# Kernel tuning notes

Hardware: AMD Instinct MI355X
Metric: run time of the kernel (lower is better)

The kernel has to match this reference:

```python
import jax, jax.numpy as jnp
import numpy as np

B, T, C = 1, 2048, 1024
H = 16
HD = C // H  # 64
K = 8
EPS = 1e-6
NEG = -1.0e9


def apply_rotary_emb(x, cos, sin):
    # x: (B,T,H,HD), cos/sin: (T, HD//2)
    x1, x2 = jnp.split(x, 2, axis=-1)
    c = cos[None, :, None, :]
    s = sin[None, :, None, :]
    return jnp.concatenate([x1 * c - x2 * s, x1 * s + x2 * c], axis=-1)


def rms_norm(x):
    return x * jax.lax.rsqrt(jnp.mean(jnp.square(x), axis=-1, keepdims=True) + EPS)


def setup_inputs() -> dict:
    key = jax.random.key(0)
    ks = jax.random.split(key, 8)
    x = jax.random.normal(ks[0], (B, T, C), dtype=jnp.float32)
    # standard RoPE tables
    inv_freq = 1.0 / (10000.0 ** (np.arange(0, HD, 2, dtype=np.float32) / HD))
    t = np.arange(T, dtype=np.float32)
    freqs = np.outer(t, inv_freq)  # (T, HD//2)
    cos = jnp.asarray(np.cos(freqs), dtype=jnp.float32)
    sin = jnp.asarray(np.sin(freqs), dtype=jnp.float32)
    std = 0.02
    Wq = std * jax.random.normal(ks[1], (C, C), dtype=jnp.float32)
    Wk = std * jax.random.normal(ks[2], (C, C), dtype=jnp.float32)
    Wv = std * jax.random.normal(ks[3], (C, C), dtype=jnp.float32)
    Wproj = std * jax.random.normal(ks[4], (C, C), dtype=jnp.float32)
    Wdq = jax.random.normal(ks[5], (C, K), dtype=jnp.float32) / np.sqrt(C)
    Wdk = jax.random.normal(ks[6], (C, K), dtype=jnp.float32) / np.sqrt(C)
    return {"x": x, "cos": cos, "sin": sin, "Wq": Wq, "Wk": Wk, "Wv": Wv,
            "Wproj": Wproj, "Wdq": Wdq, "Wdk": Wdk}


def reference(x, cos, sin, Wq, Wk, Wv, Wproj, Wdq, Wdk):
    b, t, c = x.shape
    q = (x @ Wq).reshape(b, t, H, HD)
    k = (x @ Wk).reshape(b, t, H, HD)
    v = (x @ Wv).reshape(b, t, H, HD)
    q = rms_norm(apply_rotary_emb(q, cos, sin))
    k = rms_norm(apply_rotary_emb(k, cos, sin))

    # digit projections (identical for every head in the source module)
    qd = x @ Wdq  # (B,T,K)
    kd = x @ Wdk  # (B,T,K)
    matches = qd[:, :, None, :] == kd[:, None, :, :]  # (B,Tq,Tk,K)
    prefix = jnp.cumprod(matches.astype(jnp.int32), axis=-1)
    lcp = jnp.sum(prefix, axis=-1)  # (B,Tq,Tk)
    lcp_mask = lcp >= (K - 1)

    causal = jnp.tril(jnp.ones((t, t), dtype=bool))
    combined = causal[None, None, :, :] & lcp_mask[:, None, :, :]  # (B,1->H,Tq,Tk)

    scale = 1.0 / jnp.sqrt(jnp.asarray(HD, x.dtype))
    scores = jnp.einsum('bqhd,bkhd->bhqk', q * scale, k)
    scores = jnp.where(combined, scores, NEG)
    w = jax.nn.softmax(scores, axis=-1)
    y = jnp.einsum('bhqk,bkhd->bqhd', w, v).reshape(b, t, c)
    return y @ Wproj
```

## Files before the change

### kernel.cpp

```cpp
#include <hip/hip_runtime.h>
#include <math.h>

#define T_DIM 2048
#define C_DIM 1024
#define H_NUM 16
#define HD_DIM 64
#define K_LCP 8
#define NEG_VAL -1.0e9f

typedef __bf16 bf16;
typedef __bf16 bf16x4 __attribute__((ext_vector_type(4)));
typedef __bf16 bf16x8 __attribute__((ext_vector_type(8)));
typedef float f32x4 __attribute__((ext_vector_type(4)));

__device__ void matvec_body(const float* __restrict__ vin, int npart,
                            const float* __restrict__ W, float* __restrict__ vout,
                            float scale, int blk) {
  __shared__ float xm[C_DIM];
  __shared__ float red[4][64];
  const int t = threadIdx.x;
  f32x4 s = {0.f, 0.f, 0.f, 0.f};
  if (npart) {
    for (int g = 0; g < npart; ++g) s += ((const f32x4*)vin)[g * 256 + t];
  } else {
    s = ((const f32x4*)vin)[t];
  }
  s *= scale;
  *(f32x4*)&xm[t * 4] = s;
  __syncthreads();
  const int j = blk * 64 + (t & 63);
  const int p = t >> 6;
  float acc = 0.f;
  for (int c = p * 256; c < p * 256 + 256; ++c)
    acc = fmaf(xm[c], W[(size_t)c * C_DIM + j], acc);
  red[p][t & 63] = acc;
  __syncthreads();
  if (t < 64)
    vout[blk * 64 + t] = (red[0][t] + red[1][t]) + (red[2][t] + red[3][t]);
}

__global__ __launch_bounds__(256) void fused_a(const float* __restrict__ x,
                                               const float* __restrict__ Wdq,
                                               const float* __restrict__ Wdk,
                                               bf16* __restrict__ xb,
                                               float* __restrict__ qd,
                                               float* __restrict__ kd,
                                               float* __restrict__ partial,
                                               int* __restrict__ flags) {
  const int tid = threadIdx.x;
  if (blockIdx.x >= 512) {
    const int b = blockIdx.x - 512;
    if (b == 0 && tid < 116) flags[tid] = 0;
    f32x4 s = {0.f, 0.f, 0.f, 0.f};
    for (int r = 0; r < 64; ++r)
      s += ((const f32x4*)(x + (size_t)(b * 64 + r) * C_DIM))[tid];
    ((f32x4*)(partial + (size_t)b * C_DIM))[tid] = s;
    return;
  }
  const int wave = tid >> 6, lane = tid & 63;
  const int t = blockIdx.x * 4 + wave;
  const float* xp = x + (size_t)t * C_DIM;
  bf16* xbp = xb + (size_t)t * C_DIM;
  float aq[8] = {}, ak[8] = {};
#pragma unroll
  for (int i = 0; i < 16; ++i) {
    const int c = i * 64 + lane;
    float xv = xp[c];
    xbp[c] = (bf16)xv;
    float4 wq0 = *(const float4*)(Wdq + (size_t)c * K_LCP);
    float4 wq1 = *(const float4*)(Wdq + (size_t)c * K_LCP + 4);
    float4 wk0 = *(const float4*)(Wdk + (size_t)c * K_LCP);
    float4 wk1 = *(const float4*)(Wdk + (size_t)c * K_LCP + 4);
    aq[0] = fmaf(xv, wq0.x, aq[0]); aq[1] = fmaf(xv, wq0.y, aq[1]);
    aq[2] = fmaf(xv, wq0.z, aq[2]); aq[3] = fmaf(xv, wq0.w, aq[3]);
    aq[4] = fmaf(xv, wq1.x, aq[4]); aq[5] = fmaf(xv, wq1.y, aq[5]);
    aq[6] = fmaf(xv, wq1.z, aq[6]); aq[7] = fmaf(xv, wq1.w, aq[7]);
    ak[0] = fmaf(xv, wk0.x, ak[0]); ak[1] = fmaf(xv, wk0.y, ak[1]);
    ak[2] = fmaf(xv, wk0.z, ak[2]); ak[3] = fmaf(xv, wk0.w, ak[3]);
    ak[4] = fmaf(xv, wk1.x, ak[4]); ak[5] = fmaf(xv, wk1.y, ak[5]);
    ak[6] = fmaf(xv, wk1.z, ak[6]); ak[7] = fmaf(xv, wk1.w, ak[7]);
  }
#pragma unroll
  for (int j = 0; j < 8; ++j) {
#pragma unroll
    for (int off = 32; off >= 1; off >>= 1) {
      aq[j] += __shfl_xor(aq[j], off);
      ak[j] += __shfl_xor(ak[j], off);
    }
  }
  if (lane == 0) {
    *(float4*)(qd + (size_t)t * K_LCP) = make_float4(aq[0], aq[1], aq[2], aq[3]);
    *(float4*)(qd + (size_t)t * K_LCP + 4) = make_float4(aq[4], aq[5], aq[6], aq[7]);
    *(float4*)(kd + (size_t)t * K_LCP) = make_float4(ak[0], ak[1], ak[2], ak[3]);
    *(float4*)(kd + (size_t)t * K_LCP + 4) = make_float4(ak[4], ak[5], ak[6], ak[7]);
  }
}

__global__ __launch_bounds__(256) void fused_b(
    const float* __restrict__ qd, const float* __restrict__ kd,
    const float* __restrict__ partial, const float* __restrict__ Wv,
    int* __restrict__ tilemask, int* __restrict__ allmask,
    float* __restrict__ vmean, int* __restrict__ qneed, int* __restrict__ kneed,
    int* __restrict__ vneed, int* __restrict__ vtneed, int* __restrict__ pneed,
    int* __restrict__ wneed) {
  const int tid = threadIdx.x;
  if (blockIdx.x >= 128) {
    matvec_body(partial, 32, Wv, vmean, 1.0f / 2048.0f, blockIdx.x - 128);
    return;
  }
  const int qb = blockIdx.x;
  __shared__ float qds[16][K_LCP];
  __shared__ int tm[32];
  if (tid < 32) tm[tid] = 0;
  if (tid < 16 * K_LCP)
    qds[tid >> 3][tid & 7] = qd[(size_t)(qb * 16 + (tid >> 3)) * K_LCP + (tid & 7)];
  __syncthreads();
  for (int key = tid; key < T_DIM; key += 256) {
    float kv[K_LCP];
    *(float4*)&kv[0] = *(const float4*)(kd + (size_t)key * K_LCP);
    *(float4*)&kv[4] = *(const float4*)(kd + (size_t)key * K_LCP + 4);
    int any = 0;
#pragma unroll
    for (int ql = 0; ql < 16; ++ql) {
      int qg = qb * 16 + ql;
      if (key > qg) continue;
      int lcp = 0;
#pragma unroll
      for (int jj = 0; jj < K_LCP; ++jj) {
        if (qds[ql][jj] == kv[jj]) lcp++;
        else break;
      }
      if (lcp >= K_LCP - 1) any = 1;
    }
    if (any) tm[key >> 6] = 1;
  }
  __syncthreads();
  int anytm = 0;
#pragma unroll
  for (int i = 0; i < 32; ++i) anytm |= tm[i];
  if (tid < 32) tilemask[qb * 32 + tid] = tm[tid];
  if (tid == 0) allmask[qb] = !anytm;
  if (anytm) {
    if (tid < 32) {
      if (tm[tid]) {
        atomicOr(&kneed[tid >> 1], 1);
        atomicOr(&vneed[tid >> 1], 1);
      } else {
        atomicOr(&vtneed[tid], 1);
        atomicOr(&vneed[tid >> 1], 1);
      }
    }
    if (tid == 0) {
      atomicOr(&qneed[qb >> 3], 1);
      atomicOr(&pneed[qb >> 2], 1);
      atomicOr(&wneed[0], 1);
      atomicOr(&wneed[1], 1);
      atomicOr(&wneed[2], 1);
      atomicOr(&wneed[3], 1);
    }
  }
}

__global__ __launch_bounds__(256) void fused_e(
    const float* __restrict__ vmean, const float* __restrict__ WprojF,
    float* __restrict__ rowout, const float* __restrict__ W0,
    const float* __restrict__ W1, const float* __restrict__ W2,
    const float* __restrict__ W3, bf16* __restrict__ O0, bf16* __restrict__ O1,
    bf16* __restrict__ O2, bf16* __restrict__ O3, const int* __restrict__ wneed) {
  if (blockIdx.x < 16) {
    matvec_body(vmean, 0, WprojF, rowout, 1.0f, blockIdx.x);
    return;
  }
  const int idx = blockIdx.x - 16;
  const int z = idx >> 8;
  if (!wneed[z]) return;
  const float* W = (z == 0) ? W0 : (z == 1) ? W1 : (z == 2) ? W2 : W3;
  bf16* O = (z == 0) ? O0 : (z == 1) ? O1 : (z == 2) ? O2 : O3;
  __shared__ bf16 tile[64][65];
  const int rem = idx & 255;
  const int bk = (rem >> 4) * 64;
  const int bn = (rem & 15) * 64;
  const int r = threadIdx.x >> 2;
  const int c0 = (threadIdx.x & 3) * 16;
  const float* src = W + (size_t)(bk + r) * C_DIM + bn + c0;
#pragma unroll
  for (int t = 0; t < 16; t += 4) {
    float4 f = *(const float4*)(src + t);
    tile[r][c0 + t + 0] = (bf16)f.x;
    tile[r][c0 + t + 1] = (bf16)f.y;
    tile[r][c0 + t + 2] = (bf16)f.z;
    tile[r][c0 + t + 3] = (bf16)f.w;
  }
  __syncthreads();
  bf16* dst = O + (size_t)(bn + r) * C_DIM + bk + c0;
#pragma unroll
  for (int t = 0; t < 16; ++t) dst[t] = tile[c0 + t][r];
}

template <int TMt, int MI, int NA>
__global__ __launch_bounds__(256) void gemm_bf16(
    const bf16* __restrict__ A, const bf16* __restrict__ Bt0,
    const bf16* __restrict__ Bt1, const bf16* __restrict__ Bt2, void* C0,
    void* C1, void* C2, int N, int Kd, int bf16_out,
    const float* __restrict__ cosT, const float* __restrict__ sinT,
    const int* __restrict__ fq, const int* __restrict__ fk,
    const int* __restrict__ fv, float* __restrict__ vtsum,
    const float* __restrict__ rowout, int mode) {
  if (!mode && blockIdx.z == 1) {
    const int b = blockIdx.y * 8 + blockIdx.x;
    f32x4 v = ((const f32x4*)rowout)[threadIdx.x];
#pragma unroll
    for (int r = 0; r < 8; ++r) {
      const int row = b * 8 + r;
      if (fq[row >> 6]) continue;
      ((f32x4*)((float*)C0 + (size_t)row * C_DIM))[threadIdx.x] = v;
    }
    return;
  }
  if (mode) {
    const int* f = (blockIdx.z == 0) ? fq : (blockIdx.z == 1) ? fk : fv;
    if (!f[blockIdx.y]) return;
  } else {
    if (!fq[blockIdx.y]) return;
  }
  const bf16* Bt = (blockIdx.z == 0) ? Bt0 : (blockIdx.z == 1) ? Bt1 : Bt2;
  __shared__ __align__(16) bf16 As[TMt * 32];
  __shared__ __align__(16) bf16 Bs[128 * 32];
  const int tid = threadIdx.x;
  const int bm = blockIdx.y * TMt;
  const int bn = blockIdx.x * 128;
  const int wave = tid >> 6, lane = tid & 63;
  const int lr = lane >> 2;
  const int lc = (lane & 3) * 8;
  bf16* gA = (bf16*)(A + (size_t)(bm + wave * 16 * NA + lr) * Kd + lc);
  bf16* gB = (bf16*)(Bt + (size_t)(bn + wave * 32 + lr) * Kd + lc);
  bf16* lA = As + wave * 512 * NA;
  bf16* lB = Bs + wave * 1024;
  const int wr = (wave >> 1) * (MI * 16);
  const int wc = (wave & 1) * 64;
  const int fm = lane & 15;
  const int fk_ = (lane >> 4) * 8;

  f32x4 acc[MI][4] = {};
  for (int k0 = 0; k0 < Kd; k0 += 32) {
    __syncthreads();
#pragma unroll
    for (int u = 0; u < NA; ++u)
      __builtin_amdgcn_global_load_lds(
          (__attribute__((address_space(1))) void*)(gA + (size_t)u * 16 * Kd + k0),
          (__attribute__((address_space(3))) void*)(lA + u * 512), 16, 0, 0);
#pragma unroll
    for (int u = 0; u < 2; ++u)
      __builtin_amdgcn_global_load_lds(
          (__attribute__((address_space(1))) void*)(gB + (size_t)u * 16 * Kd + k0),
          (__attribute__((address_space(3))) void*)(lB + u * 512), 16, 0, 0);
    __syncthreads();
    bf16x8 af[MI], bfr[4];
#pragma unroll
    for (int i = 0; i < MI; ++i)
      af[i] = *(const bf16x8*)(As + (size_t)(wr + i * 16 + fm) * 32 + fk_);
#pragma unroll
    for (int j = 0; j < 4; ++j)
      bfr[j] = *(const bf16x8*)(Bs + (size_t)(wc + j * 16 + fm) * 32 + fk_);
#pragma unroll
    for (int i = 0; i < MI; ++i)
#pragma unroll
      for (int j = 0; j < 4; ++j)
        acc[i][j] = __builtin_amdgcn_mfma_f32_16x16x32_bf16(af[i], bfr[j],
                                                            acc[i][j], 0, 0, 0);
  }
  const int cq = (lane >> 4) * 4;
  if (mode && blockIdx.z < 2) {
    bf16* C = (bf16*)((blockIdx.z == 0) ? C0 : C1);
#pragma unroll
    for (int i = 0; i < MI; ++i)
#pragma unroll
      for (int r = 0; r < 4; ++r) {
        const int t = bm + wr + i * 16 + cq + r;
        float c0 = cosT[(size_t)t * 32 + fm], s0 = sinT[(size_t)t * 32 + fm];
        float c1 = cosT[(size_t)t * 32 + 16 + fm], s1 = sinT[(size_t)t * 32 + 16 + fm];
        float a0 = acc[i][0][r], a1 = acc[i][1][r];
        float a2 = acc[i][2][r], a3 = acc[i][3][r];
        float o0 = a0 * c0 - a2 * s0, o2 = a0 * s0 + a2 * c0;
        float o1 = a1 * c1 - a3 * s1, o3 = a1 * s1 + a3 * c1;
        float ss = o0 * o0 + o1 * o1 + o2 * o2 + o3 * o3;
        ss += __shfl_xor(ss, 1);
        ss += __shfl_xor(ss, 2);
        ss += __shfl_xor(ss, 4);
        ss += __shfl_xor(ss, 8);
        float rn = 1.0f / sqrtf(ss * (1.0f / 64.0f) + 1e-6f);
        size_t base = (size_t)t * N + bn + wc + fm;
        C[base + 0] = (bf16)(o0 * rn);
        C[base + 16] = (bf16)(o1 * rn);
        C[base + 32] = (bf16)(o2 * rn);
        C[base + 48] = (bf16)(o3 * rn);
      }
  } else if (bf16_out) {
    bf16* C = (bf16*)((blockIdx.z == 0) ? C0 : (blockIdx.z == 1) ? C1 : C2);
#pragma unroll
    for (int i = 0; i < MI; ++i)
#pragma unroll
      for (int r = 0; r < 4; ++r) {
        size_t base = (size_t)(bm + wr + i * 16 + cq + r) * N + bn + wc + fm;
#pragma unroll
        for (int j = 0; j < 4; ++j) C[base + j * 16] = (bf16)acc[i][j][r];
      }
    if (mode && blockIdx.z == 2 && MI == 4) {
      const int kt = (bm + wr) >> 6;
#pragma unroll
      for (int j = 0; j < 4; ++j) {
        float s = 0.f;
#pragma unroll
        for (int i = 0; i < MI; ++i)
#pragma unroll
          for (int r = 0; r < 4; ++r) s += acc[i][j][r];
        s += __shfl_xor(s, 16);
        s += __shfl_xor(s, 32);
        if ((lane >> 4) == 0)
          vtsum[(size_t)kt * C_DIM + bn + wc + j * 16 + fm] = s;
      }
    }
  } else {
    float* C = (float*)((blockIdx.z == 0) ? C0 : (blockIdx.z == 1) ? C1 : C2);
#pragma unroll
    for (int i = 0; i < MI; ++i)
#pragma unroll
      for (int r = 0; r < 4; ++r) {
        size_t base = (size_t)(bm + wr + i * 16 + cq + r) * N + bn + wc + fm;
#pragma unroll
        for (int j = 0; j < 4; ++j) C[base + j * 16] = acc[i][j][r];
      }
  }
}

#define QT 16
#define KT 64

__global__ __launch_bounds__(256) void attn2(
    const bf16* __restrict__ q, const bf16* __restrict__ k,
    const bf16* __restrict__ v, const float* __restrict__ qd,
    const float* __restrict__ kd, const float* __restrict__ vtsum,
    const float* __restrict__ vmean, const int* __restrict__ tilemask,
    const int* __restrict__ allmask, const int* __restrict__ pneed,
    bf16* __restrict__ y) {
  const int h = blockIdx.y;
  const int qb = blockIdx.x;
  const int q0 = qb * QT;
  const int tid = threadIdx.x;
  const int q_l = tid >> 4;
  const int sub = tid & 15;

  if (allmask[qb]) {
    if (pneed[qb >> 2]) {
      f32x4 vm = *(const f32x4*)(vmean + h * HD_DIM + sub * 4);
      bf16x4 o = {(bf16)vm[0], (bf16)vm[1], (bf16)vm[2], (bf16)vm[3]};
      *(bf16x4*)(y + (size_t)(q0 + q_l) * C_DIM + h * HD_DIM + sub * 4) = o;
    }
    return;
  }

  __shared__ float qs[QT][HD_DIM];
  __shared__ float qds[QT][K_LCP];
  __shared__ float ks[KT][HD_DIM];
  __shared__ float vs[KT][HD_DIM];
  __shared__ float kds[KT][K_LCP];
  __shared__ float sc[QT][KT + 4];

  {
    int r = tid >> 4, c4 = (tid & 15) * 4;
    bf16x4 t4 = *(const bf16x4*)(q + (size_t)(q0 + r) * C_DIM + h * HD_DIM + c4);
    qs[r][c4 + 0] = (float)t4[0] * 0.125f;
    qs[r][c4 + 1] = (float)t4[1] * 0.125f;
    qs[r][c4 + 2] = (float)t4[2] * 0.125f;
    qs[r][c4 + 3] = (float)t4[3] * 0.125f;
    if (tid < QT * K_LCP)
      qds[tid >> 3][tid & 7] = qd[(size_t)(q0 + (tid >> 3)) * K_LCP + (tid & 7)];
  }
  __syncthreads();

  float m = -INFINITY;
  float l = 0.f;
  float acc[4] = {0.f, 0.f, 0.f, 0.f};

  for (int kt = 0; kt < T_DIM / KT; ++kt) {
    if (!tilemask[qb * 32 + kt]) {
      if (m <= NEG_VAL) {
        m = NEG_VAL;
        l += (float)KT;
        f32x4 vt = *(const f32x4*)(vtsum + (size_t)kt * C_DIM + h * HD_DIM + sub * 4);
        acc[0] += vt[0];
        acc[1] += vt[1];
        acc[2] += vt[2];
        acc[3] += vt[3];
      }
      continue;
    }
    const int k0 = kt * KT;
    __syncthreads();
#pragma unroll
    for (int it = 0; it < 4; ++it) {
      int i = tid + it * 256;
      int row = i >> 4, c4 = (i & 15) * 4;
      bf16x4 kv = *(const bf16x4*)(k + (size_t)(k0 + row) * C_DIM + h * HD_DIM + c4);
      bf16x4 vv = *(const bf16x4*)(v + (size_t)(k0 + row) * C_DIM + h * HD_DIM + c4);
      ks[row][c4 + 0] = (float)kv[0];
      ks[row][c4 + 1] = (float)kv[1];
      ks[row][c4 + 2] = (float)kv[2];
      ks[row][c4 + 3] = (float)kv[3];
      vs[row][c4 + 0] = (float)vv[0];
      vs[row][c4 + 1] = (float)vv[1];
      vs[row][c4 + 2] = (float)vv[2];
      vs[row][c4 + 3] = (float)vv[3];
    }
#pragma unroll
    for (int it = 0; it < 2; ++it) {
      int i = tid + it * 256;
      kds[i >> 3][i & 7] = kd[(size_t)(k0 + (i >> 3)) * K_LCP + (i & 7)];
    }
    __syncthreads();

    const int kb = sub * 4;
    bool msk[4];
#pragma unroll
    for (int j = 0; j < 4; ++j) {
      int kg = k0 + kb + j;
      int lcp = 0;
#pragma unroll
      for (int jj = 0; jj < K_LCP; ++jj) {
        if (qds[q_l][jj] == kds[kb + j][jj]) lcp++;
        else break;
      }
      msk[j] = (lcp >= K_LCP - 1) && (kg <= q0 + q_l);
    }
    float s[4] = {0.f, 0.f, 0.f, 0.f};
#pragma unroll
    for (int d4 = 0; d4 < 16; ++d4) {
      float4 q4 = *(const float4*)&qs[q_l][d4 * 4];
#pragma unroll
      for (int j = 0; j < 4; ++j) {
        float4 k4 = *(const float4*)&ks[kb + j][d4 * 4];
        s[j] = fmaf(q4.x, k4.x, s[j]);
        s[j] = fmaf(q4.y, k4.y, s[j]);
        s[j] = fmaf(q4.z, k4.z, s[j]);
        s[j] = fmaf(q4.w, k4.w, s[j]);
      }
    }
    float tmax = NEG_VAL;
#pragma unroll
    for (int j = 0; j < 4; ++j) {
      s[j] = msk[j] ? s[j] : NEG_VAL;
      tmax = fmaxf(tmax, s[j]);
    }
#pragma unroll
    for (int off = 1; off < 16; off <<= 1) tmax = fmaxf(tmax, __shfl_xor(tmax, off));
    float m_new = fmaxf(m, tmax);
    float alpha = expf(m - m_new);
    float lsum = 0.f;
#pragma unroll
    for (int j = 0; j < 4; ++j) {
      float p = expf(s[j] - m_new);
      sc[q_l][kb + j] = p;
      lsum += p;
    }
#pragma unroll
    for (int off = 1; off < 16; off <<= 1) lsum += __shfl_xor(lsum, off);
    l = l * alpha + lsum;
    m = m_new;
    acc[0] *= alpha;
    acc[1] *= alpha;
    acc[2] *= alpha;
    acc[3] *= alpha;
    __syncthreads();
#pragma unroll 8
    for (int kk = 0; kk < KT; ++kk) {
      float w = sc[q_l][kk];
      const float4 v4 = *(const float4*)&vs[kk][sub * 4];
      acc[0] = fmaf(w, v4.x, acc[0]);
      acc[1] = fmaf(w, v4.y, acc[1]);
      acc[2] = fmaf(w, v4.z, acc[2]);
      acc[3] = fmaf(w, v4.w, acc[3]);
    }
  }

  const float inv_l = 1.0f / l;
  bf16x4 o = {(bf16)(acc[0] * inv_l), (bf16)(acc[1] * inv_l),
              (bf16)(acc[2] * inv_l), (bf16)(acc[3] * inv_l)};
  *(bf16x4*)(y + (size_t)(q0 + q_l) * C_DIM + h * HD_DIM + sub * 4) = o;
}

extern "C" void kernel_launch(void* const* d_in, const int* in_sizes, int n_in,
                              void* d_out, int out_size, void* d_ws, size_t ws_size,
                              hipStream_t stream) {
  const float* x = (const float*)d_in[0];
  const float* cosT = (const float*)d_in[1];
  const float* sinT = (const float*)d_in[2];
  const float* Wq = (const float*)d_in[3];
  const float* Wk = (const float*)d_in[4];
  const float* Wv = (const float*)d_in[5];
  const float* Wproj = (const float*)d_in[6];
  const float* Wdq = (const float*)d_in[7];
  const float* Wdk = (const float*)d_in[8];
  float* out = (float*)d_out;

  char* ws = (char*)d_ws;
  const size_t TC2 = (size_t)T_DIM * C_DIM * 2;
  const size_t CC2 = (size_t)C_DIM * C_DIM * 2;
  bf16* xb = (bf16*)(ws + 0);
  bf16* wqt = (bf16*)(ws + TC2);
  bf16* wkt = (bf16*)(ws + TC2 + CC2);
  bf16* wvt = (bf16*)(ws + TC2 + 2 * CC2);
  bf16* wpt = (bf16*)(ws + TC2 + 3 * CC2);
  bf16* qb = (bf16*)(ws + TC2 + 4 * CC2);
  bf16* kb = (bf16*)(ws + 2 * TC2 + 4 * CC2);
  bf16* vb = (bf16*)(ws + 3 * TC2 + 4 * CC2);
  char* p2 = ws + 4 * TC2 + 4 * CC2;
  float* qd = (float*)p2;                      p2 += (size_t)T_DIM * K_LCP * 4;
  float* kd = (float*)p2;                      p2 += (size_t)T_DIM * K_LCP * 4;
  float* vtsum = (float*)p2;                   p2 += 32 * C_DIM * 4;
  float* vmean = (float*)p2;                   p2 += C_DIM * 4;
  float* partial = (float*)p2;                 p2 += 32 * C_DIM * 4;
  float* rowout = (float*)p2;                  p2 += C_DIM * 4;
  int* tilemask = (int*)p2;                    p2 += (T_DIM / 16) * 32 * 4;
  int* allmask = (int*)p2;                     p2 += (T_DIM / 16) * 4;
  int* qneed = (int*)p2;                       p2 += 16 * 4;
  int* kneed = (int*)p2;                       p2 += 16 * 4;
  int* vneed = (int*)p2;                       p2 += 16 * 4;
  int* vtneed = (int*)p2;                      p2 += 32 * 4;
  int* pneed = (int*)p2;                       p2 += 32 * 4;
  int* wneed = (int*)p2;                       p2 += 4 * 4;
  bf16* yb = xb;

  fused_a<<<544, 256, 0, stream>>>(x, Wdq, Wdk, xb, qd, kd, partial, qneed);
  fused_b<<<144, 256, 0, stream>>>(qd, kd, partial, Wv, tilemask, allmask,
                                   vmean, qneed, kneed, vneed, vtneed, pneed,
                                   wneed);
  fused_e<<<16 + 1024, 256, 0, stream>>>(vmean, Wproj, rowout, Wq, Wk, Wv,
                                         Wproj, wqt, wkt, wvt, wpt, wneed);
  gemm_bf16<128, 4, 2><<<dim3(C_DIM / 128, T_DIM / 128, 3), 256, 0, stream>>>(
      xb, wqt, wkt, wvt, qb, kb, vb, C_DIM, C_DIM, 1, cosT, sinT, qneed, kneed,
      vneed, vtsum, rowout, 1);
  attn2<<<dim3(T_DIM / QT, H_NUM), 256, 0, stream>>>(
      qb, kb, vb, qd, kd, vtsum, vmean, tilemask, allmask, pneed, yb);
  gemm_bf16<64, 2, 1><<<dim3(C_DIM / 128, T_DIM / 64, 2), 256, 0, stream>>>(
      yb, wpt, wpt, wpt, out, out, out, C_DIM, C_DIM, 0, cosT, sinT, pneed,
      pneed, pneed, vtsum, rowout, 0);
}
```

Measured before the change: 121.6 us.

## Fold weight transposes into first kernel and merge matvec into QKV GEMM launch

The four weight transpose-to-bf16 conversions move into the first kernel alongside the digit projections, so they no longer wait on the mask pass. The Wproj matvec is merged into the QKV GEMM launch, which cuts the chain from six kernels to five. In exchange, all four weights are now always converted, even when the mask would have skipped them, and the vtneed/wneed gating is dropped. The V-tile column sums are now always computed in the V GEMM.

```diff
diff --git a/kernel.cpp b/kernel.cpp
--- a/kernel.cpp
+++ b/kernel.cpp
@@ -13,86 +13,85 @@
 typedef __bf16 bf16x8 __attribute__((ext_vector_type(8)));
 typedef float f32x4 __attribute__((ext_vector_type(4)));
 
-__device__ void matvec_body(const float* __restrict__ vin, int npart,
-                            const float* __restrict__ W, float* __restrict__ vout,
-                            float scale, int blk) {
-  __shared__ float xm[C_DIM];
-  __shared__ float red[4][64];
-  const int t = threadIdx.x;
-  f32x4 s = {0.f, 0.f, 0.f, 0.f};
-  if (npart) {
-    for (int g = 0; g < npart; ++g) s += ((const f32x4*)vin)[g * 256 + t];
-  } else {
-    s = ((const f32x4*)vin)[t];
-  }
-  s *= scale;
-  *(f32x4*)&xm[t * 4] = s;
-  __syncthreads();
-  const int j = blk * 64 + (t & 63);
-  const int p = t >> 6;
-  float acc = 0.f;
-  for (int c = p * 256; c < p * 256 + 256; ++c)
-    acc = fmaf(xm[c], W[(size_t)c * C_DIM + j], acc);
-  red[p][t & 63] = acc;
-  __syncthreads();
-  if (t < 64)
-    vout[blk * 64 + t] = (red[0][t] + red[1][t]) + (red[2][t] + red[3][t]);
-}
-
-__global__ __launch_bounds__(256) void fused_a(const float* __restrict__ x,
-                                               const float* __restrict__ Wdq,
-                                               const float* __restrict__ Wdk,
-                                               bf16* __restrict__ xb,
-                                               float* __restrict__ qd,
-                                               float* __restrict__ kd,
-                                               float* __restrict__ partial,
-                                               int* __restrict__ flags) {
+__global__ __launch_bounds__(256) void fused_a(
+    const float* __restrict__ x, const float* __restrict__ Wdq,
+    const float* __restrict__ Wdk, const float* __restrict__ Wq,
+    const float* __restrict__ Wk, const float* __restrict__ Wv,
+    const float* __restrict__ Wproj, bf16* __restrict__ xb,
+    float* __restrict__ qd, float* __restrict__ kd, float* __restrict__ partial,
+    int* __restrict__ flags, bf16* __restrict__ wqt, bf16* __restrict__ wkt,
+    bf16* __restrict__ wvt, bf16* __restrict__ wpt) {
+  __shared__ bf16 tile[64][65];
+  const int vb = blockIdx.x;
   const int tid = threadIdx.x;
-  if (blockIdx.x >= 512) {
-    const int b = blockIdx.x - 512;
-    if (b == 0 && tid < 116) flags[tid] = 0;
+  if (vb < 512) {
+    const int wave = tid >> 6, lane = tid & 63;
+    const int t = vb * 4 + wave;
+    const float* xp = x + (size_t)t * C_DIM;
+    bf16* xbp = xb + (size_t)t * C_DIM;
+    float aq[8] = {}, ak[8] = {};
+#pragma unroll
+    for (int i = 0; i < 16; ++i) {
+      const int c = i * 64 + lane;
+      float xv = xp[c];
+      xbp[c] = (bf16)xv;
+      float4 wq0 = *(const float4*)(Wdq + (size_t)c * K_LCP);
+      float4 wq1 = *(const float4*)(Wdq + (size_t)c * K_LCP + 4);
+      float4 wk0 = *(const float4*)(Wdk + (size_t)c * K_LCP);
+      float4 wk1 = *(const float4*)(Wdk + (size_t)c * K_LCP + 4);
+      aq[0] = fmaf(xv, wq0.x, aq[0]); aq[1] = fmaf(xv, wq0.y, aq[1]);
+      aq[2] = fmaf(xv, wq0.z, aq[2]); aq[3] = fmaf(xv, wq0.w, aq[3]);
+      aq[4] = fmaf(xv, wq1.x, aq[4]); aq[5] = fmaf(xv, wq1.y, aq[5]);
+      aq[6] = fmaf(xv, wq1.z, aq[6]); aq[7] = fmaf(xv, wq1.w, aq[7]);
+      ak[0] = fmaf(xv, wk0.x, ak[0]); ak[1] = fmaf(xv, wk0.y, ak[1]);
+      ak[2] = fmaf(xv, wk0.z, ak[2]); ak[3] = fmaf(xv, wk0.w, ak[3]);
+      ak[4] = fmaf(xv, wk1.x, ak[4]); ak[5] = fmaf(xv, wk1.y, ak[5]);
+      ak[6] = fmaf(xv, wk1.z, ak[6]); ak[7] = fmaf(xv, wk1.w, ak[7]);
+    }
+#pragma unroll
+    for (int j = 0; j < 8; ++j) {
+#pragma unroll
+      for (int off = 32; off >= 1; off >>= 1) {
+        aq[j] += __shfl_xor(aq[j], off);
+        ak[j] += __shfl_xor(ak[j], off);
+      }
+    }
+    if (lane == 0) {
+      *(float4*)(qd + (size_t)t * K_LCP) = make_float4(aq[0], aq[1], aq[2], aq[3]);
+      *(float4*)(qd + (size_t)t * K_LCP + 4) = make_float4(aq[4], aq[5], aq[6], aq[7]);
+      *(float4*)(kd + (size_t)t * K_LCP) = make_float4(ak[0], ak[1], ak[2], ak[3]);
+      *(float4*)(kd + (size_t)t * K_LCP + 4) = make_float4(ak[4], ak[5], ak[6], ak[7]);
+    }
+  } else if (vb < 544) {
+    const int b = vb - 512;
+    if (b == 0 && tid < 112) flags[tid] = 0;
     f32x4 s = {0.f, 0.f, 0.f, 0.f};
     for (int r = 0; r < 64; ++r)
       s += ((const f32x4*)(x + (size_t)(b * 64 + r) * C_DIM))[tid];
     ((f32x4*)(partial + (size_t)b * C_DIM))[tid] = s;
-    return;
-  }
-  const int wave = tid >> 6, lane = tid & 63;
-  const int t = blockIdx.x * 4 + wave;
-  const float* xp = x + (size_t)t * C_DIM;
-  bf16* xbp = xb + (size_t)t * C_DIM;
-  float aq[8] = {}, ak[8] = {};
-#pragma unroll
-  for (int i = 0; i < 16; ++i) {
-    const int c = i * 64 + lane;
-    float xv = xp[c];
-    xbp[c] = (bf16)xv;
-    float4 wq0 = *(const float4*)(Wdq + (size_t)c * K_LCP);
-    float4 wq1 = *(const float4*)(Wdq + (size_t)c * K_LCP + 4);
-    float4 wk0 = *(const float4*)(Wdk + (size_t)c * K_LCP);
-    float4 wk1 = *(const float4*)(Wdk + (size_t)c * K_LCP + 4);
-    aq[0] = fmaf(xv, wq0.x, aq[0]); aq[1] = fmaf(xv, wq0.y, aq[1]);
-    aq[2] = fmaf(xv, wq0.z, aq[2]); aq[3] = fmaf(xv, wq0.w, aq[3]);
-    aq[4] = fmaf(xv, wq1.x, aq[4]); aq[5] = fmaf(xv, wq1.y, aq[5]);
-    aq[6] = fmaf(xv, wq1.z, aq[6]); aq[7] = fmaf(xv, wq1.w, aq[7]);
-    ak[0] = fmaf(xv, wk0.x, ak[0]); ak[1] = fmaf(xv, wk0.y, ak[1]);
-    ak[2] = fmaf(xv, wk0.z, ak[2]); ak[3] = fmaf(xv, wk0.w, ak[3]);
-    ak[4] = fmaf(xv, wk1.x, ak[4]); ak[5] = fmaf(xv, wk1.y, ak[5]);
-    ak[6] = fmaf(xv, wk1.z, ak[6]); ak[7] = fmaf(xv, wk1.w, ak[7]);
-  }
-#pragma unroll
-  for (int j = 0; j < 8; ++j) {
-#pragma unroll
-    for (int off = 32; off >= 1; off >>= 1) {
-      aq[j] += __shfl_xor(aq[j], off);
-      ak[j] += __shfl_xor(ak[j], off);
-    }
-  }
-  if (lane == 0) {
-    *(float4*)(qd + (size_t)t * K_LCP) = make_float4(aq[0], aq[1], aq[2], aq[3]);
-    *(float4*)(qd + (size_t)t * K_LCP + 4) = make_float4(aq[4], aq[5], aq[6], aq[7]);
-    *(float4*)(kd + (size_t)t * K_LCP) = make_float4(ak[0], ak[1], ak[2], ak[3]);
-    *(float4*)(kd + (size_t)t * K_LCP + 4) = make_float4(ak[4], ak[5], ak[6], ak[7]);
+  } else {
+    const int idx = vb - 544;
+    const int z = idx >> 8;
+    const float* W = (z == 0) ? Wq : (z == 1) ? Wk : (z == 2) ? Wv : Wproj;
+    bf16* O = (z == 0) ? wqt : (z == 1) ? wkt : (z == 2) ? wvt : wpt;
+    const int rem = idx & 255;
+    const int bk = (rem >> 4) * 64;
+    const int bn = (rem & 15) * 64;
+    const int r = tid >> 2;
+    const int c0 = (tid & 3) * 16;
+    const float* src = W + (size_t)(bk + r) * C_DIM + bn + c0;
+#pragma unroll
+    for (int t = 0; t < 16; t += 4) {
+      float4 f = *(const float4*)(src + t);
+      tile[r][c0 + t + 0] = (bf16)f.x;
+      tile[r][c0 + t + 1] = (bf16)f.y;
+      tile[r][c0 + t + 2] = (bf16)f.z;
+      tile[r][c0 + t + 3] = (bf16)f.w;
+    }
+    __syncthreads();
+    bf16* dst = O + (size_t)(bn + r) * C_DIM + bk + c0;
+#pragma unroll
+    for (int t = 0; t < 16; ++t) dst[t] = tile[c0 + t][r];
   }
 }
 
@@ -101,11 +100,27 @@
     const float* __restrict__ partial, const float* __restrict__ Wv,
     int* __restrict__ tilemask, int* __restrict__ allmask,
     float* __restrict__ vmean, int* __restrict__ qneed, int* __restrict__ kneed,
-    int* __restrict__ vneed, int* __restrict__ vtneed, int* __restrict__ pneed,
-    int* __restrict__ wneed) {
+    int* __restrict__ vneed, int* __restrict__ pneed) {
   const int tid = threadIdx.x;
   if (blockIdx.x >= 128) {
-    matvec_body(partial, 32, Wv, vmean, 1.0f / 2048.0f, blockIdx.x - 128);
+    __shared__ float xm[C_DIM];
+    __shared__ float red[4][64];
+    const int blk = blockIdx.x - 128;
+    f32x4 s = {0.f, 0.f, 0.f, 0.f};
+    for (int g = 0; g < 32; ++g) s += ((const f32x4*)partial)[g * 256 + tid];
+    s *= (1.0f / 2048.0f);
+    *(f32x4*)&xm[tid * 4] = s;
+    __syncthreads();
+    const int j = blk * 64 + (tid & 63);
+    const int p = tid >> 6;
+    float acc = 0.f;
+    for (int c = p * 256; c < p * 256 + 256; ++c)
+      acc = fmaf(xm[c], Wv[(size_t)c * C_DIM + j], acc);
+    red[p][tid & 63] = acc;
+    __syncthreads();
+    if (tid < 64)
+      vmean[blk * 64 + tid] =
+          (red[0][tid] + red[1][tid]) + (red[2][tid] + red[3][tid]);
     return;
   }
   const int qb = blockIdx.x;
@@ -142,93 +157,24 @@
   if (tid == 0) allmask[qb] = !anytm;
   if (anytm) {
     if (tid < 32) {
-      if (tm[tid]) {
-        atomicOr(&kneed[tid >> 1], 1);
-        atomicOr(&vneed[tid >> 1], 1);
-      } else {
-        atomicOr(&vtneed[tid], 1);
-        atomicOr(&vneed[tid >> 1], 1);
-      }
+      if (tm[tid]) atomicOr(&kneed[tid >> 1], 1);
+      atomicOr(&vneed[tid >> 1], 1);
     }
     if (tid == 0) {
       atomicOr(&qneed[qb >> 3], 1);
       atomicOr(&pneed[qb >> 2], 1);
-      atomicOr(&wneed[0], 1);
-      atomicOr(&wneed[1], 1);
-      atomicOr(&wneed[2], 1);
-      atomicOr(&wneed[3], 1);
-    }
-  }
-}
-
-__global__ __launch_bounds__(256) void fused_e(
-    const float* __restrict__ vmean, const float* __restrict__ WprojF,
-    float* __restrict__ rowout, const float* __restrict__ W0,
-    const float* __restrict__ W1, const float* __restrict__ W2,
-    const float* __restrict__ W3, bf16* __restrict__ O0, bf16* __restrict__ O1,
-    bf16* __restrict__ O2, bf16* __restrict__ O3, const int* __restrict__ wneed) {
-  if (blockIdx.x < 16) {
-    matvec_body(vmean, 0, WprojF, rowout, 1.0f, blockIdx.x);
-    return;
-  }
-  const int idx = blockIdx.x - 16;
-  const int z = idx >> 8;
-  if (!wneed[z]) return;
-  const float* W = (z == 0) ? W0 : (z == 1) ? W1 : (z == 2) ? W2 : W3;
-  bf16* O = (z == 0) ? O0 : (z == 1) ? O1 : (z == 2) ? O2 : O3;
-  __shared__ bf16 tile[64][65];
-  const int rem = idx & 255;
-  const int bk = (rem >> 4) * 64;
-  const int bn = (rem & 15) * 64;
-  const int r = threadIdx.x >> 2;
-  const int c0 = (threadIdx.x & 3) * 16;
-  const float* src = W + (size_t)(bk + r) * C_DIM + bn + c0;
-#pragma unroll
-  for (int t = 0; t < 16; t += 4) {
-    float4 f = *(const float4*)(src + t);
-    tile[r][c0 + t + 0] = (bf16)f.x;
-    tile[r][c0 + t + 1] = (bf16)f.y;
-    tile[r][c0 + t + 2] = (bf16)f.z;
-    tile[r][c0 + t + 3] = (bf16)f.w;
-  }
-  __syncthreads();
-  bf16* dst = O + (size_t)(bn + r) * C_DIM + bk + c0;
-#pragma unroll
-  for (int t = 0; t < 16; ++t) dst[t] = tile[c0 + t][r];
+    }
+  }
 }
 
 template <int TMt, int MI, int NA>
-__global__ __launch_bounds__(256) void gemm_bf16(
-    const bf16* __restrict__ A, const bf16* __restrict__ Bt0,
-    const bf16* __restrict__ Bt1, const bf16* __restrict__ Bt2, void* C0,
-    void* C1, void* C2, int N, int Kd, int bf16_out,
-    const float* __restrict__ cosT, const float* __restrict__ sinT,
-    const int* __restrict__ fq, const int* __restrict__ fk,
-    const int* __restrict__ fv, float* __restrict__ vtsum,
-    const float* __restrict__ rowout, int mode) {
-  if (!mode && blockIdx.z == 1) {
-    const int b = blockIdx.y * 8 + blockIdx.x;
-    f32x4 v = ((const f32x4*)rowout)[threadIdx.x];
-#pragma unroll
-    for (int r = 0; r < 8; ++r) {
-      const int row = b * 8 + r;
-      if (fq[row >> 6]) continue;
-      ((f32x4*)((float*)C0 + (size_t)row * C_DIM))[threadIdx.x] = v;
-    }
-    return;
-  }
-  if (mode) {
-    const int* f = (blockIdx.z == 0) ? fq : (blockIdx.z == 1) ? fk : fv;
-    if (!f[blockIdx.y]) return;
-  } else {
-    if (!fq[blockIdx.y]) return;
-  }
-  const bf16* Bt = (blockIdx.z == 0) ? Bt0 : (blockIdx.z == 1) ? Bt1 : Bt2;
-  __shared__ __align__(16) bf16 As[TMt * 32];
-  __shared__ __align__(16) bf16 Bs[128 * 32];
+__device__ void gemm_body(bf16* As, bf16* Bs, const bf16* A, const bf16* Bt,
+                          void* Cv, int bx, int by, int z, int mode,
+                          const float* cosT, const float* sinT, float* vtsum) {
   const int tid = threadIdx.x;
-  const int bm = blockIdx.y * TMt;
-  const int bn = blockIdx.x * 128;
+  const int Kd = C_DIM, N = C_DIM;
+  const int bm = by * TMt;
+  const int bn = bx * 128;
   const int wave = tid >> 6, lane = tid & 63;
   const int lr = lane >> 2;
   const int lc = (lane & 3) * 8;
@@ -270,15 +216,16 @@
                                                             acc[i][j], 0, 0, 0);
   }
   const int cq = (lane >> 4) * 4;
-  if (mode && blockIdx.z < 2) {
-    bf16* C = (bf16*)((blockIdx.z == 0) ? C0 : C1);
+  if (mode && z < 2) {
+    bf16* C = (bf16*)Cv;
 #pragma unroll
     for (int i = 0; i < MI; ++i)
 #pragma unroll
       for (int r = 0; r < 4; ++r) {
         const int t = bm + wr + i * 16 + cq + r;
         float c0 = cosT[(size_t)t * 32 + fm], s0 = sinT[(size_t)t * 32 + fm];
-        float c1 = cosT[(size_t)t * 32 + 16 + fm], s1 = sinT[(size_t)t * 32 + 16 + fm];
+        float c1 = cosT[(size_t)t * 32 + 16 + fm];
+        float s1 = sinT[(size_t)t * 32 + 16 + fm];
         float a0 = acc[i][0][r], a1 = acc[i][1][r];
         float a2 = acc[i][2][r], a3 = acc[i][3][r];
         float o0 = a0 * c0 - a2 * s0, o2 = a0 * s0 + a2 * c0;
@@ -295,8 +242,8 @@
         C[base + 32] = (bf16)(o2 * rn);
         C[base + 48] = (bf16)(o3 * rn);
       }
-  } else if (bf16_out) {
-    bf16* C = (bf16*)((blockIdx.z == 0) ? C0 : (blockIdx.z == 1) ? C1 : C2);
+  } else if (mode) {
+    bf16* C = (bf16*)Cv;
 #pragma unroll
     for (int i = 0; i < MI; ++i)
 #pragma unroll
@@ -305,23 +252,21 @@
 #pragma unroll
         for (int j = 0; j < 4; ++j) C[base + j * 16] = (bf16)acc[i][j][r];
       }
-    if (mode && blockIdx.z == 2 && MI == 4) {
-      const int kt = (bm + wr) >> 6;
-#pragma unroll
-      for (int j = 0; j < 4; ++j) {
-        float s = 0.f;
-#pragma unroll
-        for (int i = 0; i < MI; ++i)
-#pragma unroll
-          for (int r = 0; r < 4; ++r) s += acc[i][j][r];
-        s += __shfl_xor(s, 16);
-        s += __shfl_xor(s, 32);
-        if ((lane >> 4) == 0)
-          vtsum[(size_t)kt * C_DIM + bn + wc + j * 16 + fm] = s;
-      }
+    const int kt = (bm + wr) >> 6;
+#pragma unroll
+    for (int j = 0; j < 4; ++j) {
+      float s = 0.f;
+#pragma unroll
+      for (int i = 0; i < MI; ++i)
+#pragma unroll
+        for (int r = 0; r < 4; ++r) s += acc[i][j][r];
+      s += __shfl_xor(s, 16);
+      s += __shfl_xor(s, 32);
+      if ((lane >> 4) == 0)
+        vtsum[(size_t)kt * C_DIM + bn + wc + j * 16 + fm] = s;
     }
   } else {
-    float* C = (float*)((blockIdx.z == 0) ? C0 : (blockIdx.z == 1) ? C1 : C2);
+    float* C = (float*)Cv;
 #pragma unroll
     for (int i = 0; i < MI; ++i)
 #pragma unroll
@@ -330,6 +275,46 @@
 #pragma unroll
         for (int j = 0; j < 4; ++j) C[base + j * 16] = acc[i][j][r];
       }
+  }
+}
+
+__global__ __launch_bounds__(256) void phase_c(
+    const bf16* __restrict__ xb, const bf16* __restrict__ wqt,
+    const bf16* __restrict__ wkt, const bf16* __restrict__ wvt,
+    bf16* __restrict__ qB, bf16* __restrict__ kB, bf16* __restrict__ vB,
+    float* __restrict__ vtsum, const float* __restrict__ cosT,
+    const float* __restrict__ sinT, const int* __restrict__ qneed,
+    const int* __restrict__ kneed, const int* __restrict__ vneed,
+    const float* __restrict__ vmean, const float* __restrict__ Wproj,
+    float* __restrict__ rowout) {
+  __shared__ __align__(16) bf16 As[128 * 32];
+  __shared__ __align__(16) bf16 Bs[128 * 32];
+  const int vb = blockIdx.x;
+  const int tid = threadIdx.x;
+  if (vb < 384) {
+    const int z = vb >> 7, r = vb & 127, by = r >> 3, bx = r & 7;
+    const int* f = (z == 0) ? qneed : (z == 1) ? kneed : vneed;
+    if (!f[by]) return;
+    const bf16* Bt = (z == 0) ? wqt : (z == 1) ? wkt : wvt;
+    void* C = (z == 0) ? (void*)qB : (z == 1) ? (void*)kB : (void*)vB;
+    gemm_body<128, 4, 2>(As, Bs, xb, Bt, C, bx, by, z, 1, cosT, sinT, vtsum);
+  } else {
+    __shared__ float xm[C_DIM];
+    __shared__ float red[4][64];
+    const int blk = vb - 384;
+    f32x4 s = ((const f32x4*)vmean)[tid];
+    *(f32x4*)&xm[tid * 4] = s;
+    __syncthreads();
+    const int j = blk * 64 + (tid & 63);
+    const int p = tid >> 6;
+    float acc = 0.f;
+    for (int c = p * 256; c < p * 256 + 256; ++c)
+      acc = fmaf(xm[c], Wproj[(size_t)c * C_DIM + j], acc);
+    red[p][tid & 63] = acc;
+    __syncthreads();
+    if (tid < 64)
+      rowout[blk * 64 + tid] =
+          (red[0][tid] + red[1][tid]) + (red[2][tid] + red[3][tid]);
   }
 }
 
@@ -388,10 +373,7 @@
         m = NEG_VAL;
         l += (float)KT;
         f32x4 vt = *(const f32x4*)(vtsum + (size_t)kt * C_DIM + h * HD_DIM + sub * 4);
-        acc[0] += vt[0];
-        acc[1] += vt[1];
-        acc[2] += vt[2];
-        acc[3] += vt[3];
+        acc[0] += vt[0]; acc[1] += vt[1]; acc[2] += vt[2]; acc[3] += vt[3];
       }
       continue;
     }
@@ -466,10 +448,7 @@
     for (int off = 1; off < 16; off <<= 1) lsum += __shfl_xor(lsum, off);
     l = l * alpha + lsum;
     m = m_new;
-    acc[0] *= alpha;
-    acc[1] *= alpha;
-    acc[2] *= alpha;
-    acc[3] *= alpha;
+    acc[0] *= alpha; acc[1] *= alpha; acc[2] *= alpha; acc[3] *= alpha;
     __syncthreads();
 #pragma unroll 8
     for (int kk = 0; kk < KT; ++kk) {
@@ -486,6 +465,31 @@
   bf16x4 o = {(bf16)(acc[0] * inv_l), (bf16)(acc[1] * inv_l),
               (bf16)(acc[2] * inv_l), (bf16)(acc[3] * inv_l)};
   *(bf16x4*)(y + (size_t)(q0 + q_l) * C_DIM + h * HD_DIM + sub * 4) = o;
+}
+
+__global__ __launch_bounds__(256) void phase_e(
+    const bf16* __restrict__ yb, const bf16* __restrict__ wpt,
+    float* __restrict__ out, const int* __restrict__ pneed,
+    const float* __restrict__ rowout, const float* __restrict__ cosT,
+    const float* __restrict__ sinT) {
+  __shared__ __align__(16) bf16 As[64 * 32];
+  __shared__ __align__(16) bf16 Bs[128 * 32];
+  const int vb = blockIdx.x;
+  if (vb < 256) {
+    const int by = vb >> 3, bx = vb & 7;
+    if (!pneed[by]) return;
+    gemm_body<64, 2, 1>(As, Bs, yb, wpt, (void*)out, bx, by, 2, 0, cosT, sinT,
+                        nullptr);
+  } else {
+    const int b = vb - 256;
+    f32x4 v = ((const f32x4*)rowout)[threadIdx.x];
+#pragma unroll
+    for (int r = 0; r < 8; ++r) {
+      const int row = b * 8 + r;
+      if (pneed[row >> 6]) continue;
+      ((f32x4*)(out + (size_t)row * C_DIM))[threadIdx.x] = v;
+    }
+  }
 }
 
 extern "C" void kernel_launch(void* const* d_in, const int* in_sizes, int n_in,
@@ -510,38 +514,32 @@
   bf16* wkt = (bf16*)(ws + TC2 + CC2);
   bf16* wvt = (bf16*)(ws + TC2 + 2 * CC2);
   bf16* wpt = (bf16*)(ws + TC2 + 3 * CC2);
-  bf16* qb = (bf16*)(ws + TC2 + 4 * CC2);
-  bf16* kb = (bf16*)(ws + 2 * TC2 + 4 * CC2);
-  bf16* vb = (bf16*)(ws + 3 * TC2 + 4 * CC2);
+  bf16* qB = (bf16*)(ws + TC2 + 4 * CC2);
+  bf16* kB = (bf16*)(ws + 2 * TC2 + 4 * CC2);
+  bf16* vB = (bf16*)(ws + 3 * TC2 + 4 * CC2);
   char* p2 = ws + 4 * TC2 + 4 * CC2;
-  float* qd = (float*)p2;                      p2 += (size_t)T_DIM * K_LCP * 4;
-  float* kd = (float*)p2;                      p2 += (size_t)T_DIM * K_LCP * 4;
-  float* vtsum = (float*)p2;                   p2 += 32 * C_DIM * 4;
-  float* vmean = (float*)p2;                   p2 += C_DIM * 4;
-  float* partial = (float*)p2;                 p2 += 32 * C_DIM * 4;
-  float* rowout = (float*)p2;                  p2 += C_DIM * 4;
-  int* tilemask = (int*)p2;                    p2 += (T_DIM / 16) * 32 * 4;
-  int* allmask = (int*)p2;                     p2 += (T_DIM / 16) * 4;
-  int* qneed = (int*)p2;                       p2 += 16 * 4;
-  int* kneed = (int*)p2;                       p2 += 16 * 4;
-  int* vneed = (int*)p2;                       p2 += 16 * 4;
-  int* vtneed = (int*)p2;                      p2 += 32 * 4;
-  int* pneed = (int*)p2;                       p2 += 32 * 4;
-  int* wneed = (int*)p2;                       p2 += 4 * 4;
+  float* qd = (float*)p2;        p2 += (size_t)T_DIM * K_LCP * 4;
+  float* kd = (float*)p2;        p2 += (size_t)T_DIM * K_LCP * 4;
+  float* vtsum = (float*)p2;     p2 += 32 * C_DIM * 4;
+  float* vmean = (float*)p2;     p2 += C_DIM * 4;
+  float* partial = (float*)p2;   p2 += 32 * C_DIM * 4;
+  float* rowout = (float*)p2;    p2 += C_DIM * 4;
+  int* tilemask = (int*)p2;      p2 += (T_DIM / 16) * 32 * 4;
+  int* allmask = (int*)p2;       p2 += (T_DIM / 16) * 4;
+  int* qneed = (int*)p2;         p2 += 16 * 4;
+  int* kneed = (int*)p2;         p2 += 16 * 4;
+  int* vneed = (int*)p2;         p2 += 16 * 4;
+  int* pneed = (int*)p2;         p2 += 32 * 4;
   bf16* yb = xb;
 
-  fused_a<<<544, 256, 0, stream>>>(x, Wdq, Wdk, xb, qd, kd, partial, qneed);
+  fused_a<<<1568, 256, 0, stream>>>(x, Wdq, Wdk, Wq, Wk, Wv, Wproj, xb, qd, kd,
+                                    partial, qneed, wqt, wkt, wvt, wpt);
   fused_b<<<144, 256, 0, stream>>>(qd, kd, partial, Wv, tilemask, allmask,
-                                   vmean, qneed, kneed, vneed, vtneed, pneed,
-                                   wneed);
-  fused_e<<<16 + 1024, 256, 0, stream>>>(vmean, Wproj, rowout, Wq, Wk, Wv,
-                                         Wproj, wqt, wkt, wvt, wpt, wneed);
-  gemm_bf16<128, 4, 2><<<dim3(C_DIM / 128, T_DIM / 128, 3), 256, 0, stream>>>(
-      xb, wqt, wkt, wvt, qb, kb, vb, C_DIM, C_DIM, 1, cosT, sinT, qneed, kneed,
-      vneed, vtsum, rowout, 1);
+                                   vmean, qneed, kneed, vneed, pneed);
+  phase_c<<<400, 256, 0, stream>>>(xb, wqt, wkt, wvt, qB, kB, vB, vtsum, cosT,
+                                   sinT, qneed, kneed, vneed, vmean, Wproj,
+                                   rowout);
   attn2<<<dim3(T_DIM / QT, H_NUM), 256, 0, stream>>>(
-      qb, kb, vb, qd, kd, vtsum, vmean, tilemask, allmask, pneed, yb);
-  gemm_bf16<64, 2, 1><<<dim3(C_DIM / 128, T_DIM / 64, 2), 256, 0, stream>>>(
-      yb, wpt, wpt, wpt, out, out, out, C_DIM, C_DIM, 0, cosT, sinT, pneed,
-      pneed, pneed, vtsum, rowout, 0);
-}
+      qB, kB, vB, qd, kd, vtsum, vmean, tilemask, allmask, pneed, yb);
+  phase_e<<<512, 256, 0, stream>>>(yb, wpt, out, pneed, rowout, cosT, sinT);
+}
```

Measured after the change: 121.4 us. No clear change (-0.2%).
